# Performance work log

Hardware: AMD Instinct MI355X
Metric: run time of the kernel (lower is better)

The kernel has to match this reference:

```python
import jax, jax.numpy as jnp
import numpy as np

PATCH = 768
POS = 64
HID = 512
B, N = 8, 2048


def setup_inputs() -> dict:
    key = jax.random.key(0)
    ks = jax.random.split(key, 8)
    d_in = PATCH + POS
    s = 1.0 / np.sqrt(d_in)
    return {
        "patches": jax.random.normal(ks[0], (B, N, PATCH), jnp.float32),
        "positions": jax.random.normal(ks[1], (B, N, POS), jnp.float32),
        "Wq": jax.random.uniform(ks[2], (d_in, HID), jnp.float32, -s, s),
        "bq": jax.random.uniform(ks[3], (HID,), jnp.float32, -s, s),
        "Wk": jax.random.uniform(ks[4], (d_in, HID), jnp.float32, -s, s),
        "bk": jax.random.uniform(ks[5], (d_in and HID,), jnp.float32, -s, s),
        "Wv": jax.random.uniform(ks[6], (d_in, HID), jnp.float32, -s, s),
        "bv": jax.random.uniform(ks[7], (HID,), jnp.float32, -s, s),
    }


def reference(patches, positions, Wq, bq, Wk, bk, Wv, bv):
    # concat patch features with positional features: [B, N, PATCH+POS]
    x = jnp.concatenate([patches, positions], axis=-1)
    Q = x @ Wq + bq  # [B, N, HID]
    K = x @ Wk + bk
    V = x @ Wv + bv
    scale = jnp.sqrt(jnp.asarray(HID, x.dtype))
    scores = jnp.einsum("bnd,bmd->bnm", Q, K) / scale  # [B, N, N]
    weights = jax.nn.softmax(scores, axis=-1)
    return jnp.einsum("bnm,bmd->bnd", weights, V)  # [B, N, HID]
```

## Files before the change

### kernel.cpp

```cpp
#include <hip/hip_runtime.h>
#include <hip/hip_bf16.h>
#include <math.h>

typedef __hip_bfloat16 bf16;
typedef __attribute__((ext_vector_type(4))) float f32x4;
typedef __attribute__((ext_vector_type(8))) short s16x8;

typedef const __attribute__((address_space(1))) void gvoid_t;
typedef __attribute__((address_space(3))) void lvoid_t;

__device__ __forceinline__ void gload16(const void* g, void* l) {
  __builtin_amdgcn_global_load_lds((gvoid_t*)g, (lvoid_t*)l, 16, 0, 0);
}
__device__ __forceinline__ unsigned short f2b(float f) {
  bf16 h = __float2bfloat16(f);
  return *(unsigned short*)&h;
}

__global__ __launch_bounds__(256) void prep_x(const float* __restrict__ patches,
                                              const float* __restrict__ positions,
                                              bf16* __restrict__ xb) {
  const long long row = blockIdx.x;
  const int c = threadIdx.x;
  const bool lo = (c < 192);
  const bool hi = (c >= 192) && (c < 208);
  const float* src = lo ? (patches + row * 768 + c * 4)
                        : (positions + row * 64 + (c - 192) * 4);
  if (lo || hi) {
    float4 v = *(const float4*)src;
    const int dst = lo ? (c * 4) : (768 + (c - 192) * 4);
    uint2 w;
    w.x = (unsigned int)f2b(v.x) | ((unsigned int)f2b(v.y) << 16);
    w.y = (unsigned int)f2b(v.z) | ((unsigned int)f2b(v.w) << 16);
    *(uint2*)(xb + row * 832 + dst) = w;
  }
}

__global__ __launch_bounds__(256) void prep_w(const float* __restrict__ Wq,
                                              const float* __restrict__ Wk,
                                              const float* __restrict__ Wv,
                                              bf16* __restrict__ Wt) {
  __shared__ float tile[32][33];
  const int z = blockIdx.z;
  const float* W = (z == 0) ? Wq : (z == 1) ? Wk : Wv;
  bf16* T = Wt + (long long)z * 512 * 832;
  const int n0 = blockIdx.x * 32;
  const int k0 = blockIdx.y * 32;
  const int tx = threadIdx.x, ty = threadIdx.y;
  #pragma unroll
  for (int i = 0; i < 32; i += 8)
    tile[ty + i][tx] = W[(long long)(k0 + ty + i) * 512 + n0 + tx];
  __syncthreads();
  #pragma unroll
  for (int i = 0; i < 32; i += 8)
    T[(long long)(n0 + ty + i) * 832 + k0 + tx] = __float2bfloat16(tile[tx][ty + i]);
}

__global__ __launch_bounds__(256) void gemm_qkv(
    const bf16* __restrict__ xb, const bf16* __restrict__ Wt,
    const float* __restrict__ bq, const float* __restrict__ bk,
    const float* __restrict__ bv,
    bf16* __restrict__ qk, bf16* __restrict__ vt) {
  __shared__ bf16 As[128 * 64];
  __shared__ bf16 Bs[128 * 64];
  const int tid = threadIdx.x;
  const int wave = tid >> 6, lane = tid & 63;
  const int llo = lane & 15, lhi = lane >> 4;
  const int wm = wave >> 1, wn = wave & 1;

  const unsigned int lin = blockIdx.x;
  const unsigned int xcd = lin & 7u, idx = lin >> 3;
  const unsigned int g = xcd * 192u + idx;
  const unsigned int bm_t = g / 12u;
  const unsigned int bn_t = g - bm_t * 12u;
  const int row0 = (int)bm_t * 128;
  const int col0 = (int)bn_t * 128;
  const int z = col0 >> 9;

  f32x4 acc[4][4] = {};

  for (int kt = 0; kt < 832; kt += 64) {
    #pragma unroll
    for (int i = 0; i < 4; i++) {
      const int c = i * 256 + tid;
      const int r = c >> 3, cc = c & 7;
      const int kk = (cc ^ (r & 7)) << 3;
      gload16(xb + ((long long)(row0 + r) * 832 + kt + kk),
              (char*)As + (long long)(i * 256 + wave * 64) * 16);
      gload16(Wt + ((long long)(col0 + r) * 832 + kt + kk),
              (char*)Bs + (long long)(i * 256 + wave * 64) * 16);
    }
    __syncthreads();
    #pragma unroll
    for (int k0 = 0; k0 < 64; k0 += 32) {
      const int xk = ((((k0 >> 3) + lhi) ^ (llo & 7)) << 3);
      s16x8 af[4], bfr[4];
      #pragma unroll
      for (int mf = 0; mf < 4; mf++)
        af[mf] = *(const s16x8*)&As[(wm * 64 + mf * 16 + llo) * 64 + xk];
      #pragma unroll
      for (int nf = 0; nf < 4; nf++)
        bfr[nf] = *(const s16x8*)&Bs[(wn * 64 + nf * 16 + llo) * 64 + xk];
      #pragma unroll
      for (int mf = 0; mf < 4; mf++)
        #pragma unroll
        for (int nf = 0; nf < 4; nf++)
          acc[mf][nf] = __builtin_amdgcn_mfma_f32_16x16x32_bf16(
              af[mf], bfr[nf], acc[mf][nf], 0, 0, 0);
    }
    __syncthreads();
  }

  if (z < 2) {
    const float* bias = z ? bk : bq;
    bf16* outp = qk + (long long)z * 16384 * 512;
    #pragma unroll
    for (int mf = 0; mf < 4; mf++)
      #pragma unroll
      for (int nf = 0; nf < 4; nf++) {
        const int c = (col0 & 511) + wn * 64 + nf * 16 + llo;
        const int grow0 = row0 + wm * 64 + mf * 16 + lhi * 4;
        const float bb = bias[c];
        #pragma unroll
        for (int r = 0; r < 4; r++)
          outp[(long long)(grow0 + r) * 512 + c] =
              __float2bfloat16(acc[mf][nf][r] + bb);
      }
  } else {
    #pragma unroll
    for (int mf = 0; mf < 4; mf++)
      #pragma unroll
      for (int nf = 0; nf < 4; nf++) {
        const int c = (col0 & 511) + wn * 64 + nf * 16 + llo;
        const int grow0 = row0 + wm * 64 + mf * 16 + lhi * 4;
        const int b = grow0 >> 11, j = grow0 & 2047;
        const float bb = bv[c];
        uint2 w;
        w.x = (unsigned int)f2b(acc[mf][nf][0] + bb) |
              ((unsigned int)f2b(acc[mf][nf][1] + bb) << 16);
        w.y = (unsigned int)f2b(acc[mf][nf][2] + bb) |
              ((unsigned int)f2b(acc[mf][nf][3] + bb) << 16);
        *(uint2*)(vt + (long long)b * 512 * 2048 + (long long)c * 2048 + j) = w;
      }
  }
}

__global__ __launch_bounds__(256) void gemm_scores(const bf16* __restrict__ qk,
                                                   bf16* __restrict__ S,
                                                   float* __restrict__ rowsumP) {
  __shared__ bf16 As[128 * 64];
  __shared__ bf16 Bs[128 * 64];
  __shared__ float psum[4][64];
  const int tid = threadIdx.x;
  const int wave = tid >> 6, lane = tid & 63;
  const int llo = lane & 15, lhi = lane >> 4;
  const int wm = wave >> 1, wn = wave & 1;

  const unsigned int lin = blockIdx.x;
  const unsigned int xcd = lin & 7u, idx = lin >> 3;
  const unsigned int g = xcd * 256u + idx;
  const int b = (int)(g >> 8);
  const unsigned int rem = g & 255u;
  const int row0 = (int)(rem >> 4) * 128;
  const int coltile = (int)(rem & 15u);
  const int col0 = coltile * 128;

  const bf16* Ab = qk + (long long)b * 2048 * 512;
  const bf16* Bb = qk + (long long)16384 * 512 + (long long)b * 2048 * 512;

  f32x4 acc[4][4] = {};
  for (int kt = 0; kt < 512; kt += 64) {
    #pragma unroll
    for (int i = 0; i < 4; i++) {
      const int c = i * 256 + tid;
      const int r = c >> 3, cc = c & 7;
      const int kk = (cc ^ (r & 7)) << 3;
      gload16(Ab + ((long long)(row0 + r) * 512 + kt + kk),
              (char*)As + (long long)(i * 256 + wave * 64) * 16);
      gload16(Bb + ((long long)(col0 + r) * 512 + kt + kk),
              (char*)Bs + (long long)(i * 256 + wave * 64) * 16);
    }
    __syncthreads();
    #pragma unroll
    for (int k0 = 0; k0 < 64; k0 += 32) {
      const int xk = ((((k0 >> 3) + lhi) ^ (llo & 7)) << 3);
      s16x8 af[4], bfr[4];
      #pragma unroll
      for (int mf = 0; mf < 4; mf++)
        af[mf] = *(const s16x8*)&As[(wm * 64 + mf * 16 + llo) * 64 + xk];
      #pragma unroll
      for (int nf = 0; nf < 4; nf++)
        bfr[nf] = *(const s16x8*)&Bs[(wn * 64 + nf * 16 + llo) * 64 + xk];
      #pragma unroll
      for (int mf = 0; mf < 4; mf++)
        #pragma unroll
        for (int nf = 0; nf < 4; nf++)
          acc[mf][nf] = __builtin_amdgcn_mfma_f32_16x16x32_bf16(
              af[mf], bfr[nf], acc[mf][nf], 0, 0, 0);
    }
    __syncthreads();
  }

  const float alpha = 0.044194173824159216f;
  #pragma unroll
  for (int mf = 0; mf < 4; mf++)
    #pragma unroll
    for (int nf = 0; nf < 4; nf++)
      #pragma unroll
      for (int r = 0; r < 4; r++)
        acc[mf][nf][r] = __expf(acc[mf][nf][r] * alpha);

  bf16* Sb = S + (long long)b * 2048 * 2048;
  #pragma unroll
  for (int mf = 0; mf < 4; mf++)
    #pragma unroll
    for (int nf = 0; nf < 4; nf++) {
      const int gcol = col0 + wn * 64 + nf * 16 + llo;
      const int grow0 = row0 + wm * 64 + mf * 16 + lhi * 4;
      #pragma unroll
      for (int r = 0; r < 4; r++)
        Sb[(long long)(grow0 + r) * 2048 + gcol] =
            __float2bfloat16(acc[mf][nf][r]);
    }

  #pragma unroll
  for (int mf = 0; mf < 4; mf++) {
    #pragma unroll
    for (int r = 0; r < 4; r++) {
      float p = acc[mf][0][r] + acc[mf][1][r] + acc[mf][2][r] + acc[mf][3][r];
      p += __shfl_xor(p, 1, 64);
      p += __shfl_xor(p, 2, 64);
      p += __shfl_xor(p, 4, 64);
      p += __shfl_xor(p, 8, 64);
      if (llo == 0) psum[wave][mf * 16 + lhi * 4 + r] = p;
    }
  }
  __syncthreads();
  if (tid < 128) {
    const int wmx = tid >> 6, i = tid & 63;
    const float v = psum[wmx * 2][i] + psum[wmx * 2 + 1][i];
    rowsumP[((long long)(b * 16 + coltile)) * 2048 + row0 + wmx * 64 + i] = v;
  }
}

__global__ __launch_bounds__(256) void reduce_rowsum(
    const float* __restrict__ rowsumP, float* __restrict__ rinv) {
  const int i = blockIdx.x * 256 + threadIdx.x;
  const int b = i >> 11, row = i & 2047;
  const float* p = rowsumP + ((long long)b * 16) * 2048 + row;
  float s = 0.f;
  #pragma unroll
  for (int t = 0; t < 16; t++) s += p[t * 2048];
  rinv[i] = 1.0f / s;
}

__global__ __launch_bounds__(256) void gemm_pv(const bf16* __restrict__ S,
                                               const bf16* __restrict__ vt,
                                               const float* __restrict__ rinv,
                                               float* __restrict__ out) {
  __shared__ bf16 As[128 * 64];
  __shared__ bf16 Bs[128 * 64];
  const int tid = threadIdx.x;
  const int wave = tid >> 6, lane = tid & 63;
  const int llo = lane & 15, lhi = lane >> 4;
  const int wm = wave >> 1, wn = wave & 1;

  const unsigned int lin = blockIdx.x;
  const unsigned int xcd = lin & 7u, idx = lin >> 3;
  const int b = (int)xcd;
  const int row0 = (int)(idx >> 2) * 128;
  const int col0 = (int)(idx & 3u) * 128;

  const bf16* Ab = S + (long long)b * 2048 * 2048;
  const bf16* Bb = vt + (long long)b * 512 * 2048;

  f32x4 acc[4][4] = {};
  for (int kt = 0; kt < 2048; kt += 64) {
    #pragma unroll
    for (int i = 0; i < 4; i++) {
      const int c = i * 256 + tid;
      const int r = c >> 3, cc = c & 7;
      const int kk = (cc ^ (r & 7)) << 3;
      gload16(Ab + ((long long)(row0 + r) * 2048 + kt + kk),
              (char*)As + (long long)(i * 256 + wave * 64) * 16);
      gload16(Bb + ((long long)(col0 + r) * 2048 + kt + kk),
              (char*)Bs + (long long)(i * 256 + wave * 64) * 16);
    }
    __syncthreads();
    #pragma unroll
    for (int k0 = 0; k0 < 64; k0 += 32) {
      const int xk = ((((k0 >> 3) + lhi) ^ (llo & 7)) << 3);
      s16x8 af[4], bfr[4];
      #pragma unroll
      for (int mf = 0; mf < 4; mf++)
        af[mf] = *(const s16x8*)&As[(wm * 64 + mf * 16 + llo) * 64 + xk];
      #pragma unroll
      for (int nf = 0; nf < 4; nf++)
        bfr[nf] = *(const s16x8*)&Bs[(wn * 64 + nf * 16 + llo) * 64 + xk];
      #pragma unroll
      for (int mf = 0; mf < 4; mf++)
        #pragma unroll
        for (int nf = 0; nf < 4; nf++)
          acc[mf][nf] = __builtin_amdgcn_mfma_f32_16x16x32_bf16(
              af[mf], bfr[nf], acc[mf][nf], 0, 0, 0);
    }
    __syncthreads();
  }

  const float* rs = rinv + (long long)b * 2048;
  float* Ob = out + (long long)b * 2048 * 512;
  #pragma unroll
  for (int mf = 0; mf < 4; mf++) {
    const int grow0 = row0 + wm * 64 + mf * 16 + lhi * 4;
    float iv[4];
    #pragma unroll
    for (int r = 0; r < 4; r++) iv[r] = rs[grow0 + r];
    #pragma unroll
    for (int nf = 0; nf < 4; nf++) {
      const int gcol = col0 + wn * 64 + nf * 16 + llo;
      #pragma unroll
      for (int r = 0; r < 4; r++)
        Ob[(long long)(grow0 + r) * 512 + gcol] = acc[mf][nf][r] * iv[r];
    }
  }
}

extern "C" void kernel_launch(void* const* d_in, const int* in_sizes, int n_in,
                              void* d_out, int out_size, void* d_ws, size_t ws_size,
                              hipStream_t stream) {
  const float* patches = (const float*)d_in[0];
  const float* positions = (const float*)d_in[1];
  const float* Wq = (const float*)d_in[2];
  const float* bq = (const float*)d_in[3];
  const float* Wk = (const float*)d_in[4];
  const float* bk = (const float*)d_in[5];
  const float* Wv = (const float*)d_in[6];
  const float* bv = (const float*)d_in[7];
  float* out = (float*)d_out;

  if (ws_size < 149422080u) return;

  char* ws = (char*)d_ws;
  bf16* Wt = (bf16*)(ws);
  bf16* xb = (bf16*)(ws + 2555904);
  bf16* qk = (bf16*)(ws + 29818880);
  bf16* vt = (bf16*)(ws + 63373312);
  bf16* S  = (bf16*)(ws + 80150528);
  float* rinv    = (float*)(ws + 147259392);
  float* rowsumP = (float*)(ws + 147324928);

  prep_x<<<16384, 256, 0, stream>>>(patches, positions, xb);
  prep_w<<<dim3(16, 26, 3), dim3(32, 8), 0, stream>>>(Wq, Wk, Wv, Wt);
  gemm_qkv<<<1536, 256, 0, stream>>>(xb, Wt, bq, bk, bv, qk, vt);
  gemm_scores<<<2048, 256, 0, stream>>>(qk, S, rowsumP);
  reduce_rowsum<<<64, 256, 0, stream>>>(rowsumP, rinv);
  gemm_pv<<<512, 256, 0, stream>>>(S, vt, rinv, out);
}
```

Before: 274.6 us.

## Switch GEMMs to 32x32x16 MFMA and fold rowsum reduction into PV kernel

All three GEMM kernels move from 16x16x32 to 32x32x16 bf16 MFMA tiles, with a new LDS XOR swizzle that matches the 32-row fragment access pattern. The separate reduce_rowsum launch is removed: gemm_pv now sums the partial row sums for its 128 rows into shared memory and applies the reciprocal in its epilogue. The aim is fewer LDS fragment reads per MFMA and one less kernel launch. In exchange, every gemm_pv block redundantly re-reads the row-sum partials. The 32-row output layout also makes epilogue stores less contiguous.

```diff
diff --git a/kernel.cpp b/kernel.cpp
--- a/kernel.cpp
+++ b/kernel.cpp
@@ -3,7 +3,7 @@
 #include <math.h>
 
 typedef __hip_bfloat16 bf16;
-typedef __attribute__((ext_vector_type(4))) float f32x4;
+typedef __attribute__((ext_vector_type(16))) float f32x16;
 typedef __attribute__((ext_vector_type(8))) short s16x8;
 
 typedef const __attribute__((address_space(1))) void gvoid_t;
@@ -16,6 +16,7 @@
   bf16 h = __float2bfloat16(f);
   return *(unsigned short*)&h;
 }
+__device__ __forceinline__ int swz(int r) { return (r ^ (r >> 3)) & 7; }
 
 __global__ __launch_bounds__(256) void prep_x(const float* __restrict__ patches,
                                               const float* __restrict__ positions,
@@ -65,7 +66,7 @@
   __shared__ bf16 Bs[128 * 64];
   const int tid = threadIdx.x;
   const int wave = tid >> 6, lane = tid & 63;
-  const int llo = lane & 15, lhi = lane >> 4;
+  const int l31 = lane & 31, l5 = lane >> 5;
   const int wm = wave >> 1, wn = wave & 1;
 
   const unsigned int lin = blockIdx.x;
@@ -77,14 +78,14 @@
   const int col0 = (int)bn_t * 128;
   const int z = col0 >> 9;
 
-  f32x4 acc[4][4] = {};
+  f32x16 acc[2][2] = {};
 
   for (int kt = 0; kt < 832; kt += 64) {
     #pragma unroll
     for (int i = 0; i < 4; i++) {
       const int c = i * 256 + tid;
       const int r = c >> 3, cc = c & 7;
-      const int kk = (cc ^ (r & 7)) << 3;
+      const int kk = (cc ^ swz(r)) << 3;
       gload16(xb + ((long long)(row0 + r) * 832 + kt + kk),
               (char*)As + (long long)(i * 256 + wave * 64) * 16);
       gload16(Wt + ((long long)(col0 + r) * 832 + kt + kk),
@@ -92,21 +93,24 @@
     }
     __syncthreads();
     #pragma unroll
-    for (int k0 = 0; k0 < 64; k0 += 32) {
-      const int xk = ((((k0 >> 3) + lhi) ^ (llo & 7)) << 3);
-      s16x8 af[4], bfr[4];
-      #pragma unroll
-      for (int mf = 0; mf < 4; mf++)
-        af[mf] = *(const s16x8*)&As[(wm * 64 + mf * 16 + llo) * 64 + xk];
-      #pragma unroll
-      for (int nf = 0; nf < 4; nf++)
-        bfr[nf] = *(const s16x8*)&Bs[(wn * 64 + nf * 16 + llo) * 64 + xk];
-      #pragma unroll
-      for (int mf = 0; mf < 4; mf++)
-        #pragma unroll
-        for (int nf = 0; nf < 4; nf++)
-          acc[mf][nf] = __builtin_amdgcn_mfma_f32_16x16x32_bf16(
-              af[mf], bfr[nf], acc[mf][nf], 0, 0, 0);
+    for (int s = 0; s < 4; s++) {
+      s16x8 af[2], bfr[2];
+      #pragma unroll
+      for (int mt = 0; mt < 2; mt++) {
+        const int row = wm * 64 + mt * 32 + l31;
+        af[mt] = *(const s16x8*)&As[row * 64 + (((s * 2 + l5) ^ swz(row)) << 3)];
+      }
+      #pragma unroll
+      for (int nt = 0; nt < 2; nt++) {
+        const int row = wn * 64 + nt * 32 + l31;
+        bfr[nt] = *(const s16x8*)&Bs[row * 64 + (((s * 2 + l5) ^ swz(row)) << 3)];
+      }
+      #pragma unroll
+      for (int mt = 0; mt < 2; mt++)
+        #pragma unroll
+        for (int nt = 0; nt < 2; nt++)
+          acc[mt][nt] = __builtin_amdgcn_mfma_f32_32x32x16_bf16(
+              af[mt], bfr[nt], acc[mt][nt], 0, 0, 0);
     }
     __syncthreads();
   }
@@ -115,32 +119,38 @@
     const float* bias = z ? bk : bq;
     bf16* outp = qk + (long long)z * 16384 * 512;
     #pragma unroll
-    for (int mf = 0; mf < 4; mf++)
-      #pragma unroll
-      for (int nf = 0; nf < 4; nf++) {
-        const int c = (col0 & 511) + wn * 64 + nf * 16 + llo;
-        const int grow0 = row0 + wm * 64 + mf * 16 + lhi * 4;
+    for (int mt = 0; mt < 2; mt++)
+      #pragma unroll
+      for (int nt = 0; nt < 2; nt++) {
+        const int c = (col0 & 511) + wn * 64 + nt * 32 + l31;
         const float bb = bias[c];
-        #pragma unroll
-        for (int r = 0; r < 4; r++)
-          outp[(long long)(grow0 + r) * 512 + c] =
-              __float2bfloat16(acc[mf][nf][r] + bb);
+        const int gb = row0 + wm * 64 + mt * 32 + 4 * l5;
+        #pragma unroll
+        for (int reg = 0; reg < 16; reg++) {
+          const int grow = gb + (reg & 3) + 8 * (reg >> 2);
+          outp[(long long)grow * 512 + c] =
+              __float2bfloat16(acc[mt][nt][reg] + bb);
+        }
       }
   } else {
     #pragma unroll
-    for (int mf = 0; mf < 4; mf++)
-      #pragma unroll
-      for (int nf = 0; nf < 4; nf++) {
-        const int c = (col0 & 511) + wn * 64 + nf * 16 + llo;
-        const int grow0 = row0 + wm * 64 + mf * 16 + lhi * 4;
-        const int b = grow0 >> 11, j = grow0 & 2047;
+    for (int mt = 0; mt < 2; mt++)
+      #pragma unroll
+      for (int nt = 0; nt < 2; nt++) {
+        const int c = (col0 & 511) + wn * 64 + nt * 32 + l31;
         const float bb = bv[c];
-        uint2 w;
-        w.x = (unsigned int)f2b(acc[mf][nf][0] + bb) |
-              ((unsigned int)f2b(acc[mf][nf][1] + bb) << 16);
-        w.y = (unsigned int)f2b(acc[mf][nf][2] + bb) |
-              ((unsigned int)f2b(acc[mf][nf][3] + bb) << 16);
-        *(uint2*)(vt + (long long)b * 512 * 2048 + (long long)c * 2048 + j) = w;
+        const int gb = row0 + wm * 64 + mt * 32 + 4 * l5;
+        #pragma unroll
+        for (int hi = 0; hi < 4; hi++) {
+          const int rr = gb + 8 * hi;
+          const int b = rr >> 11, j = rr & 2047;
+          uint2 w;
+          w.x = (unsigned int)f2b(acc[mt][nt][hi * 4 + 0] + bb) |
+                ((unsigned int)f2b(acc[mt][nt][hi * 4 + 1] + bb) << 16);
+          w.y = (unsigned int)f2b(acc[mt][nt][hi * 4 + 2] + bb) |
+                ((unsigned int)f2b(acc[mt][nt][hi * 4 + 3] + bb) << 16);
+          *(uint2*)(vt + (long long)b * 512 * 2048 + (long long)c * 2048 + j) = w;
+        }
       }
   }
 }
@@ -153,7 +163,7 @@
   __shared__ float psum[4][64];
   const int tid = threadIdx.x;
   const int wave = tid >> 6, lane = tid & 63;
-  const int llo = lane & 15, lhi = lane >> 4;
+  const int l31 = lane & 31, l5 = lane >> 5;
   const int wm = wave >> 1, wn = wave & 1;
 
   const unsigned int lin = blockIdx.x;
@@ -168,13 +178,13 @@
   const bf16* Ab = qk + (long long)b * 2048 * 512;
   const bf16* Bb = qk + (long long)16384 * 512 + (long long)b * 2048 * 512;
 
-  f32x4 acc[4][4] = {};
+  f32x16 acc[2][2] = {};
   for (int kt = 0; kt < 512; kt += 64) {
     #pragma unroll
     for (int i = 0; i < 4; i++) {
       const int c = i * 256 + tid;
       const int r = c >> 3, cc = c & 7;
-      const int kk = (cc ^ (r & 7)) << 3;
+      const int kk = (cc ^ swz(r)) << 3;
       gload16(Ab + ((long long)(row0 + r) * 512 + kt + kk),
               (char*)As + (long long)(i * 256 + wave * 64) * 16);
       gload16(Bb + ((long long)(col0 + r) * 512 + kt + kk),
@@ -182,59 +192,64 @@
     }
     __syncthreads();
     #pragma unroll
-    for (int k0 = 0; k0 < 64; k0 += 32) {
-      const int xk = ((((k0 >> 3) + lhi) ^ (llo & 7)) << 3);
-      s16x8 af[4], bfr[4];
-      #pragma unroll
-      for (int mf = 0; mf < 4; mf++)
-        af[mf] = *(const s16x8*)&As[(wm * 64 + mf * 16 + llo) * 64 + xk];
-      #pragma unroll
-      for (int nf = 0; nf < 4; nf++)
-        bfr[nf] = *(const s16x8*)&Bs[(wn * 64 + nf * 16 + llo) * 64 + xk];
-      #pragma unroll
-      for (int mf = 0; mf < 4; mf++)
-        #pragma unroll
-        for (int nf = 0; nf < 4; nf++)
-          acc[mf][nf] = __builtin_amdgcn_mfma_f32_16x16x32_bf16(
-              af[mf], bfr[nf], acc[mf][nf], 0, 0, 0);
+    for (int s = 0; s < 4; s++) {
+      s16x8 af[2], bfr[2];
+      #pragma unroll
+      for (int mt = 0; mt < 2; mt++) {
+        const int row = wm * 64 + mt * 32 + l31;
+        af[mt] = *(const s16x8*)&As[row * 64 + (((s * 2 + l5) ^ swz(row)) << 3)];
+      }
+      #pragma unroll
+      for (int nt = 0; nt < 2; nt++) {
+        const int row = wn * 64 + nt * 32 + l31;
+        bfr[nt] = *(const s16x8*)&Bs[row * 64 + (((s * 2 + l5) ^ swz(row)) << 3)];
+      }
+      #pragma unroll
+      for (int mt = 0; mt < 2; mt++)
+        #pragma unroll
+        for (int nt = 0; nt < 2; nt++)
+          acc[mt][nt] = __builtin_amdgcn_mfma_f32_32x32x16_bf16(
+              af[mt], bfr[nt], acc[mt][nt], 0, 0, 0);
     }
     __syncthreads();
   }
 
   const float alpha = 0.044194173824159216f;
   #pragma unroll
-  for (int mf = 0; mf < 4; mf++)
-    #pragma unroll
-    for (int nf = 0; nf < 4; nf++)
-      #pragma unroll
-      for (int r = 0; r < 4; r++)
-        acc[mf][nf][r] = __expf(acc[mf][nf][r] * alpha);
+  for (int mt = 0; mt < 2; mt++)
+    #pragma unroll
+    for (int nt = 0; nt < 2; nt++)
+      #pragma unroll
+      for (int reg = 0; reg < 16; reg++)
+        acc[mt][nt][reg] = __expf(acc[mt][nt][reg] * alpha);
 
   bf16* Sb = S + (long long)b * 2048 * 2048;
   #pragma unroll
-  for (int mf = 0; mf < 4; mf++)
-    #pragma unroll
-    for (int nf = 0; nf < 4; nf++) {
-      const int gcol = col0 + wn * 64 + nf * 16 + llo;
-      const int grow0 = row0 + wm * 64 + mf * 16 + lhi * 4;
-      #pragma unroll
-      for (int r = 0; r < 4; r++)
-        Sb[(long long)(grow0 + r) * 2048 + gcol] =
-            __float2bfloat16(acc[mf][nf][r]);
-    }
-
-  #pragma unroll
-  for (int mf = 0; mf < 4; mf++) {
-    #pragma unroll
-    for (int r = 0; r < 4; r++) {
-      float p = acc[mf][0][r] + acc[mf][1][r] + acc[mf][2][r] + acc[mf][3][r];
+  for (int mt = 0; mt < 2; mt++)
+    #pragma unroll
+    for (int nt = 0; nt < 2; nt++) {
+      const int gcol = col0 + wn * 64 + nt * 32 + l31;
+      const int gb = row0 + wm * 64 + mt * 32 + 4 * l5;
+      #pragma unroll
+      for (int reg = 0; reg < 16; reg++) {
+        const int grow = gb + (reg & 3) + 8 * (reg >> 2);
+        Sb[(long long)grow * 2048 + gcol] = __float2bfloat16(acc[mt][nt][reg]);
+      }
+    }
+
+  #pragma unroll
+  for (int mt = 0; mt < 2; mt++)
+    #pragma unroll
+    for (int reg = 0; reg < 16; reg++) {
+      float p = acc[mt][0][reg] + acc[mt][1][reg];
       p += __shfl_xor(p, 1, 64);
       p += __shfl_xor(p, 2, 64);
       p += __shfl_xor(p, 4, 64);
       p += __shfl_xor(p, 8, 64);
-      if (llo == 0) psum[wave][mf * 16 + lhi * 4 + r] = p;
-    }
-  }
+      p += __shfl_xor(p, 16, 64);
+      if (l31 == 0)
+        psum[wave][mt * 32 + (reg & 3) + 8 * (reg >> 2) + 4 * l5] = p;
+    }
   __syncthreads();
   if (tid < 128) {
     const int wmx = tid >> 6, i = tid & 63;
@@ -243,26 +258,16 @@
   }
 }
 
-__global__ __launch_bounds__(256) void reduce_rowsum(
-    const float* __restrict__ rowsumP, float* __restrict__ rinv) {
-  const int i = blockIdx.x * 256 + threadIdx.x;
-  const int b = i >> 11, row = i & 2047;
-  const float* p = rowsumP + ((long long)b * 16) * 2048 + row;
-  float s = 0.f;
-  #pragma unroll
-  for (int t = 0; t < 16; t++) s += p[t * 2048];
-  rinv[i] = 1.0f / s;
-}
-
 __global__ __launch_bounds__(256) void gemm_pv(const bf16* __restrict__ S,
                                                const bf16* __restrict__ vt,
-                                               const float* __restrict__ rinv,
+                                               const float* __restrict__ rowsumP,
                                                float* __restrict__ out) {
   __shared__ bf16 As[128 * 64];
   __shared__ bf16 Bs[128 * 64];
+  __shared__ float rinvL[128];
   const int tid = threadIdx.x;
   const int wave = tid >> 6, lane = tid & 63;
-  const int llo = lane & 15, lhi = lane >> 4;
+  const int l31 = lane & 31, l5 = lane >> 5;
   const int wm = wave >> 1, wn = wave & 1;
 
   const unsigned int lin = blockIdx.x;
@@ -271,16 +276,24 @@
   const int row0 = (int)(idx >> 2) * 128;
   const int col0 = (int)(idx & 3u) * 128;
 
+  if (tid < 128) {
+    const float* rp = rowsumP + ((long long)b * 16) * 2048 + row0 + tid;
+    float s = 0.f;
+    #pragma unroll
+    for (int t = 0; t < 16; t++) s += rp[t * 2048];
+    rinvL[tid] = 1.0f / s;
+  }
+
   const bf16* Ab = S + (long long)b * 2048 * 2048;
   const bf16* Bb = vt + (long long)b * 512 * 2048;
 
-  f32x4 acc[4][4] = {};
+  f32x16 acc[2][2] = {};
   for (int kt = 0; kt < 2048; kt += 64) {
     #pragma unroll
     for (int i = 0; i < 4; i++) {
       const int c = i * 256 + tid;
       const int r = c >> 3, cc = c & 7;
-      const int kk = (cc ^ (r & 7)) << 3;
+      const int kk = (cc ^ swz(r)) << 3;
       gload16(Ab + ((long long)(row0 + r) * 2048 + kt + kk),
               (char*)As + (long long)(i * 256 + wave * 64) * 16);
       gload16(Bb + ((long long)(col0 + r) * 2048 + kt + kk),
@@ -288,41 +301,41 @@
     }
     __syncthreads();
     #pragma unroll
-    for (int k0 = 0; k0 < 64; k0 += 32) {
-      const int xk = ((((k0 >> 3) + lhi) ^ (llo & 7)) << 3);
-      s16x8 af[4], bfr[4];
-      #pragma unroll
-      for (int mf = 0; mf < 4; mf++)
-        af[mf] = *(const s16x8*)&As[(wm * 64 + mf * 16 + llo) * 64 + xk];
-      #pragma unroll
-      for (int nf = 0; nf < 4; nf++)
-        bfr[nf] = *(const s16x8*)&Bs[(wn * 64 + nf * 16 + llo) * 64 + xk];
-      #pragma unroll
-      for (int mf = 0; mf < 4; mf++)
-        #pragma unroll
-        for (int nf = 0; nf < 4; nf++)
-          acc[mf][nf] = __builtin_amdgcn_mfma_f32_16x16x32_bf16(
-              af[mf], bfr[nf], acc[mf][nf], 0, 0, 0);
-    }
-    __syncthreads();
-  }
-
-  const float* rs = rinv + (long long)b * 2048;
+    for (int s = 0; s < 4; s++) {
+      s16x8 af[2], bfr[2];
+      #pragma unroll
+      for (int mt = 0; mt < 2; mt++) {
+        const int row = wm * 64 + mt * 32 + l31;
+        af[mt] = *(const s16x8*)&As[row * 64 + (((s * 2 + l5) ^ swz(row)) << 3)];
+      }
+      #pragma unroll
+      for (int nt = 0; nt < 2; nt++) {
+        const int row = wn * 64 + nt * 32 + l31;
+        bfr[nt] = *(const s16x8*)&Bs[row * 64 + (((s * 2 + l5) ^ swz(row)) << 3)];
+      }
+      #pragma unroll
+      for (int mt = 0; mt < 2; mt++)
+        #pragma unroll
+        for (int nt = 0; nt < 2; nt++)
+          acc[mt][nt] = __builtin_amdgcn_mfma_f32_32x32x16_bf16(
+              af[mt], bfr[nt], acc[mt][nt], 0, 0, 0);
+    }
+    __syncthreads();
+  }
+
   float* Ob = out + (long long)b * 2048 * 512;
   #pragma unroll
-  for (int mf = 0; mf < 4; mf++) {
-    const int grow0 = row0 + wm * 64 + mf * 16 + lhi * 4;
-    float iv[4];
-    #pragma unroll
-    for (int r = 0; r < 4; r++) iv[r] = rs[grow0 + r];
-    #pragma unroll
-    for (int nf = 0; nf < 4; nf++) {
-      const int gcol = col0 + wn * 64 + nf * 16 + llo;
-      #pragma unroll
-      for (int r = 0; r < 4; r++)
-        Ob[(long long)(grow0 + r) * 512 + gcol] = acc[mf][nf][r] * iv[r];
-    }
-  }
+  for (int mt = 0; mt < 2; mt++)
+    #pragma unroll
+    for (int nt = 0; nt < 2; nt++) {
+      const int gcol = col0 + wn * 64 + nt * 32 + l31;
+      const int gb = wm * 64 + mt * 32 + 4 * l5;
+      #pragma unroll
+      for (int reg = 0; reg < 16; reg++) {
+        const int rl = gb + (reg & 3) + 8 * (reg >> 2);
+        Ob[(long long)(row0 + rl) * 512 + gcol] = acc[mt][nt][reg] * rinvL[rl];
+      }
+    }
 }
 
 extern "C" void kernel_launch(void* const* d_in, const int* in_sizes, int n_in,
@@ -338,7 +351,7 @@
   const float* bv = (const float*)d_in[7];
   float* out = (float*)d_out;
 
-  if (ws_size < 149422080u) return;
+  if (ws_size < 149356544u) return;
 
   char* ws = (char*)d_ws;
   bf16* Wt = (bf16*)(ws);
@@ -346,13 +359,11 @@
   bf16* qk = (bf16*)(ws + 29818880);
   bf16* vt = (bf16*)(ws + 63373312);
   bf16* S  = (bf16*)(ws + 80150528);
-  float* rinv    = (float*)(ws + 147259392);
-  float* rowsumP = (float*)(ws + 147324928);
+  float* rowsumP = (float*)(ws + 147259392);
 
   prep_x<<<16384, 256, 0, stream>>>(patches, positions, xb);
   prep_w<<<dim3(16, 26, 3), dim3(32, 8), 0, stream>>>(Wq, Wk, Wv, Wt);
   gemm_qkv<<<1536, 256, 0, stream>>>(xb, Wt, bq, bk, bv, qk, vt);
   gemm_scores<<<2048, 256, 0, stream>>>(qk, S, rowsumP);
-  reduce_rowsum<<<64, 256, 0, stream>>>(rowsumP, rinv);
-  gemm_pv<<<512, 256, 0, stream>>>(S, vt, rinv, out);
-}
+  gemm_pv<<<512, 256, 0, stream>>>(S, vt, rowsumP, out);
+}
```

After: 275.5 us. No clear change (+0.3%).
